# Performance work log

Measured on AMD Instinct MI355X. Metric: run time of the kernel, lower is better.

## Reference

```python
import math
import jax
import jax.numpy as jnp
import numpy as np

LMAX = 6                 # lmax
F8, F2 = 16, 64          # f_out//8, f_out//2 for f_out=128
DIM6 = sum((2 * l + 1) ** 2 for l in range(LMAX + 1))  # 455 = dim of so3_irreps(6)
NA = NB = NG = 16        # SO(3) activation grid (alpha, beta, gamma)
B, T, H, C = 32, 16, 4, 128


def _real_sh(lmax, xyz):
    # real spherical harmonics: (N,3) unit vectors -> (N,(lmax+1)^2), m=-l..l per l
    x, y, z = xyz[:, 0], xyz[:, 1], xyz[:, 2]
    st = np.sqrt(np.clip(1.0 - z * z, 0.0, None))
    phi = np.arctan2(y, x)
    n = xyz.shape[0]
    P = np.zeros((lmax + 1, lmax + 1, n))
    P[0, 0] = 1.0
    for m in range(1, lmax + 1):
        P[m, m] = -(2 * m - 1) * st * P[m - 1, m - 1]
    for m in range(lmax):
        P[m + 1, m] = (2 * m + 1) * z * P[m, m]
    for m in range(lmax + 1):
        for l in range(m + 2, lmax + 1):
            P[l, m] = ((2 * l - 1) * z * P[l - 1, m] - (l + m - 1) * P[l - 2, m]) / (l - m)
    cols = []
    for l in range(lmax + 1):
        for m in range(-l, l + 1):
            am = abs(m)
            K = math.sqrt((2 * l + 1) / (4 * math.pi) * math.factorial(l - am) / math.factorial(l + am))
            if m > 0:
                cols.append(math.sqrt(2.0) * K * np.cos(m * phi) * P[l, m])
            elif m < 0:
                cols.append(math.sqrt(2.0) * K * np.sin(am * phi) * P[l, am])
            else:
                cols.append(K * P[l, 0])
    return np.stack(cols, axis=-1)


def _flat_wigner(lmax, Rs):
    # component-normalized flat real Wigner-D basis: (G,3,3) -> (G, sum_l (2l+1)^2)
    # D_l(R) solved from Y_l(R x) = D_l(R) Y_l(x) by least squares in float64
    rng = np.random.default_rng(0)
    pts = rng.normal(size=(32, 3))
    pts /= np.linalg.norm(pts, axis=1, keepdims=True)
    Y = _real_sh(lmax, pts)                                     # (32,(lmax+1)^2)
    rp = np.einsum('gij,nj->gni', Rs, pts).reshape(-1, 3)
    Yr = _real_sh(lmax, rp).reshape(len(Rs), 32, -1)            # (G,32,(lmax+1)^2)
    blocks = []
    for l in range(lmax + 1):
        d = 2 * l + 1
        o = l * l
        Apinv = np.linalg.pinv(Y[:, o:o + d])                   # (d,32)
        D = np.einsum('kn,gnm->gmk', Apinv, Yr[:, :, o:o + d])  # (G,d,d)
        blocks.append(math.sqrt(d) * D.reshape(len(Rs), d * d))
    return np.concatenate(blocks, axis=-1)


def _rz(a):
    c, s = np.cos(a), np.sin(a)
    z, o = np.zeros_like(a), np.ones_like(a)
    return np.stack([np.stack([c, -s, z], -1), np.stack([s, c, z], -1), np.stack([z, z, o], -1)], -2)


def _ry(a):
    c, s = np.cos(a), np.sin(a)
    z, o = np.zeros_like(a), np.ones_like(a)
    return np.stack([np.stack([c, z, s], -1), np.stack([z, o, z], -1), np.stack([-s, z, c], -1)], -2)


def _so3_grid():
    # ZYZ Euler grid, Gauss-Legendre in beta; rotations (G,3,3) + Haar weights (G,) summing to 1
    nodes, wts = np.polynomial.legendre.leggauss(NB)
    betas = np.arccos(nodes)
    alphas = np.arange(NA) * 2 * np.pi / NA
    gammas = np.arange(NG) * 2 * np.pi / NG
    Aa, Bb, Cg = np.meshgrid(alphas, betas, gammas, indexing='ij')
    Rs = _rz(Aa.ravel()) @ _ry(Bb.ravel()) @ _rz(Cg.ravel())
    w = np.broadcast_to(wts[None, :, None], (NA, NB, NG)).ravel().copy()
    w *= (2 * np.pi / NA) * (2 * np.pi / NG) / (8 * np.pi ** 2)
    return Rs, w


def _ico_rotations():
    # the 60 rotations of the icosahedral group, generated by closure
    phi = (1.0 + 5.0 ** 0.5) / 2.0
    def rot(axis, ang):
        a = np.asarray(axis, dtype=np.float64)
        a = a / np.linalg.norm(a)
        K = np.array([[0.0, -a[2], a[1]], [a[2], 0.0, -a[0]], [-a[1], a[0], 0.0]])
        return np.eye(3) + math.sin(ang) * K + (1.0 - math.cos(ang)) * (K @ K)
    gens = [rot([0.0, 1.0, phi], 2.0 * np.pi / 5.0), rot([0.0, 0.0, 1.0], np.pi)]
    elems = [np.eye(3)]
    seen = {tuple(np.round(np.eye(3), 5).ravel())}
    frontier = list(elems)
    while frontier:
        nxt = []
        for R in frontier:
            for g in gens:
                Q = g @ R
                k = tuple(np.round(Q, 5).ravel())
                if k not in seen:
                    seen.add(k)
                    elems.append(Q)
                    nxt.append(Q)
        frontier = nxt
    return np.stack(elems)


def _equi_linear(xl, wl):
    # e3nn-style per-irrep linear: xl (...,f_in,u,m), wl (f_in,f_out,u,v); fan_in = f_in*u
    fan_in = wl.shape[0] * wl.shape[2]
    return jnp.einsum('...fum,fguv->...gvm', xl, wl) / np.sqrt(fan_in)


def _forward(x, trajectory, w1s, w1v, w2, D_in, D_outw, ico_wigners):
    b, t, _ = trajectory.shape
    # pack '1x0e+3x1e': scalar = traj[...,9], vectors = traj[...,:9]
    s = trajectory[..., 9][..., None, None, None]       # (b,t,f=1,u=1,m=1)
    v = trajectory[..., :9].reshape(b, t, 1, 3, 3)      # (b,t,f=1,u=3,m=3)
    h = jnp.concatenate([_equi_linear(s, w1s).reshape(b, t, F8, 1),
                         _equi_linear(v, w1v).reshape(b, t, F8, 9)], axis=-1)  # (b,t,16,10)
    # SO(3) activation: coeffs -> grid signal -> relu -> coeffs (lmax 1 -> 6)
    sig = jax.nn.relu(jnp.einsum('btci,gi->btcg', h, D_in))
    h = jnp.einsum('btcg,gi->btci', sig, D_outw)        # (b,t,16,455)
    # per-l equivariant linear, f 16 -> 64
    outs = []
    o = 0
    for l in range(LMAX + 1):
        d = 2 * l + 1
        xl = h[..., o:o + d * d].reshape(b, t, F8, d, d)
        outs.append(_equi_linear(xl, w2[l]).reshape(b, t, F2, d * d))
        o += d * d
    traj = jnp.concatenate(outs, axis=-1)               # (b,t,64,455)
    traj = jnp.einsum('bhcj,ij->bhci', traj, ico_wigners)  # sample on ico rotations
    xg = jnp.einsum('bhcj,ij->bhci', x, ico_wigners)
    return xg, traj


def setup_inputs():
    key = jax.random.key(0)
    ks = jax.random.split(key, 11)
    Rs, w = _so3_grid()
    D_in = _flat_wigner(1, Rs).astype(np.float32)                      # (G,10)
    D_outw = (_flat_wigner(LMAX, Rs) * w[:, None]).astype(np.float32)  # (G,455)
    ico = _flat_wigner(LMAX, _ico_rotations()).astype(np.float32)      # (60,455)
    inp = dict(
        x=jax.random.normal(ks[0], (B, H, C, DIM6), jnp.float32),
        trajectory=jax.random.normal(ks[1], (B, T, 10), jnp.float32),
        w1s=jax.random.normal(ks[2], (1, F8, 1, 1), jnp.float32),
        w1v=jax.random.normal(ks[3], (1, F8, 3, 3), jnp.float32),
        D_in=jnp.asarray(D_in),
        D_outw=jnp.asarray(D_outw),
        ico_wigners=jnp.asarray(ico),
    )
    for l in range(LMAX + 1):
        inp['w2_%d' % l] = jax.random.normal(ks[4 + l], (F8, F2, 2 * l + 1, 2 * l + 1), jnp.float32)
    return inp


def reference(x, trajectory, w1s, w1v, w2_0, w2_1, w2_2, w2_3, w2_4, w2_5, w2_6, D_in, D_outw, ico_wigners):
    w2 = [w2_0, w2_1, w2_2, w2_3, w2_4, w2_5, w2_6]
    return _forward(x, trajectory, w1s, w1v, w2, D_in, D_outw, ico_wigners)
```

## Files before the change

### kernel.cpp

```cpp
#include <hip/hip_runtime.h>
#include <math.h>


#define NBT  512
#define F8c  16
#define F2c  64
#define GJ   455
#define GG   4096
#define NICO 60
#define JP   512

typedef short bf16x8 __attribute__((ext_vector_type(8)));
typedef float f32x4  __attribute__((ext_vector_type(4)));
typedef unsigned int u32;
typedef unsigned short ushort;

struct W7 { const float* p[7]; };

__device__ __forceinline__ ushort f2bf(float f) {
  u32 u = __float_as_uint(f);
  return (ushort)((u + 0x7fffu + ((u >> 16) & 1u)) >> 16);
}

__device__ __forceinline__ int sel7(int l, int a0, int a1, int a2, int a3,
                                    int a4, int a5, int a6) {
  int r = a6;
  r = (l == 5) ? a5 : r; r = (l == 4) ? a4 : r; r = (l == 3) ? a3 : r;
  r = (l == 2) ? a2 : r; r = (l == 1) ? a1 : r; r = (l == 0) ? a0 : r;
  return r;
}
__device__ __forceinline__ float sel7f(int l, float a0, float a1, float a2,
                                       float a3, float a4, float a5, float a6) {
  float r = a6;
  r = (l == 5) ? a5 : r; r = (l == 4) ? a4 : r; r = (l == 3) ? a3 : r;
  r = (l == 2) ? a2 : r; r = (l == 1) ? a1 : r; r = (l == 0) ? a0 : r;
  return r;
}

__global__ __launch_bounds__(256) void k_pre(const float* __restrict__ traj,
                                             const float* __restrict__ w1s,
                                             const float* __restrict__ w1v,
                                             const float* __restrict__ ico,
                                             const float* __restrict__ Dout,
                                             W7 w2,
                                             float* __restrict__ h,
                                             ushort* __restrict__ icoB,
                                             ushort* __restrict__ icoBx,
                                             ushort* __restrict__ DoutBT,
                                             ushort* __restrict__ Abuf,
                                             ushort* __restrict__ Bbuf) {
  __shared__ float t[64][65];
  int b = blockIdx.x, tid = threadIdx.x;
  if (b < 2240) {
    ((uint4*)Abuf)[b * 256 + tid] = (uint4){0, 0, 0, 0};
  } else if (b < 2752) {
    int b2 = b - 2240;
    int jt = b2 & 7, kt = b2 >> 3;
    int tx = tid & 63, ty = tid >> 6;
    #pragma unroll
    for (int i = 0; i < 16; ++i) {
      int r = i * 4 + ty, j = jt * 64 + tx;
      t[r][tx] = (j < GJ) ? Dout[(size_t)(kt * 64 + r) * GJ + j] : 0.f;
    }
    __syncthreads();
    #pragma unroll
    for (int i = 0; i < 16; ++i) {
      int jl = i * 4 + ty;
      DoutBT[(size_t)(jt * 64 + jl) * GG + kt * 64 + tx] = f2bf(t[tx][jl]);
    }
  } else if (b < 4992) {
    int ee = (b - 2752) * 256 + tid;
    if (ee < 573440) {
      int l = (ee >= 4096) + (ee >= 16384) + (ee >= 57344) + (ee >= 114688) +
              (ee >= 225280) + (ee >= 360448);
      int base = sel7(l, 0, 4096, 16384, 57344, 114688, 225280, 360448);
      int d    = sel7(l, 1, 3, 5, 7, 9, 11, 13);
      int Kp   = sel7(l, 64, 64, 128, 128, 192, 192, 256);
      int local = ee - base;
      int row = local / Kp, kcol = local - row * Kp;
      int g2 = row / d, v = row - g2 * d;
      ushort val = 0;
      if (kcol < 16 * d) {
        int f = kcol / d, u = kcol - f * d;
        const float* wl = w2.p[l];
        float scl = rsqrtf(16.f * (float)d);
        val = f2bf(wl[(((size_t)f * 64 + g2) * d + u) * d + v] * scl);
      }
      Bbuf[ee] = val;
    }
  } else if (b < 5312) {
    int idx = (b - 4992) * 256 + tid;
    if (idx < NBT * 160) {
      int bt = idx / 160, r = idx % 160, c = r / 10, i = r % 10;
      const float* tr = traj + bt * 10;
      float val;
      if (i == 0) {
        val = tr[9] * w1s[c];
      } else {
        int k = i - 1, v = k / 3, m = k % 3;
        float s = 0.f;
        #pragma unroll
        for (int u = 0; u < 3; ++u) s = fmaf(tr[u * 3 + m], w1v[c * 9 + u * 3 + v], s);
        val = s * 0.57735026918962576f;
      }
      h[idx] = val;
    }
  } else if (b < 5440) {
    int e = (b - 5312) * 256 + tid;
    int i = e >> 9, k = e & 511;
    ushort val = 0;
    if (i < NICO && k < GJ) {
      int l = (k >= 1) + (k >= 10) + (k >= 35) + (k >= 84) + (k >= 165) + (k >= 286);
      int o = sel7(l, 0, 1, 10, 35, 84, 165, 286);
      int d = sel7(l, 1, 3, 5, 7, 9, 11, 13);
      float rcpd = sel7f(l, 1.f, 1.f / 3.f, 0.2f, 1.f / 7.f, 1.f / 9.f,
                         1.f / 11.f, 1.f / 13.f);
      int local = k - o;
      int m = (int)(((float)local + 0.5f) * rcpd);
      int v = local - m * d;
      val = f2bf(ico[i * GJ + o + v * d + m]);
    }
    icoB[e] = val;
  } else {
    int e = (b - 5440) * 256 + tid;
    int i = e >> 9, j = e & 511;
    icoBx[e] = (i < NICO && j < GJ) ? f2bf(ico[i * GJ + j]) : (ushort)0;
  }
}

__global__ __launch_bounds__(256) void k_sig(const float* __restrict__ h,
                                             const float* __restrict__ Din,
                                             ushort* __restrict__ sigb) {
  __shared__ float hs[160];
  int tid = threadIdx.x;
  int mb = blockIdx.y;
  int kt = blockIdx.x;
  if (tid < 160) hs[tid] = h[mb * 160 + tid];
  float dr[80];
  const float4* dp = (const float4*)(Din + (size_t)(kt * 2048 + tid * 8) * 10);
  #pragma unroll
  for (int q = 0; q < 20; ++q) {
    float4 v = dp[q];
    dr[q * 4 + 0] = v.x; dr[q * 4 + 1] = v.y; dr[q * 4 + 2] = v.z; dr[q * 4 + 3] = v.w;
  }
  __syncthreads();
  #pragma unroll
  for (int r = 0; r < 16; ++r) {
    float hv[10];
    #pragma unroll
    for (int i = 0; i < 10; ++i) hv[i] = hs[r * 10 + i];
    bf16x8 o;
    #pragma unroll
    for (int j = 0; j < 8; ++j) {
      float s = 0.f;
      #pragma unroll
      for (int i = 0; i < 10; ++i) s = fmaf(hv[i], dr[j * 10 + i], s);
      o[j] = (short)f2bf(fmaxf(s, 0.f));
    }
    *(bf16x8*)&sigb[((size_t)(mb * 16 + r)) * GG + kt * 2048 + tid * 8] = o;
  }
}

__global__ __launch_bounds__(256) void k_mm2s(const ushort* __restrict__ A,
                                              const ushort* __restrict__ Bm,
                                              float* __restrict__ part) {
  __shared__ __align__(16) short Asb[2][128 * 64];
  __shared__ __align__(16) short Bsb[2][128 * 64];
  int tid = threadIdx.x;
  int lane = tid & 63, wid = tid >> 6;
  int quad = lane >> 4, lr = lane & 15;
  int wm = wid >> 1, wn = wid & 1;
  int bid = blockIdx.x;
  int mb = bid & 63;
  int split = (bid >> 6) & 1;
  int nb = bid >> 7;
  int k0 = split * 2048;

  const ushort* Ab = A + (size_t)mb * 128 * GG + k0;
  const ushort* Bb = Bm + (size_t)nb * 128 * GG + k0;

  f32x4 acc[4][4];
  #pragma unroll
  for (int a = 0; a < 4; ++a)
    #pragma unroll
    for (int b = 0; b < 4; ++b) acc[a][b] = (f32x4){0.f, 0.f, 0.f, 0.f};

  auto stage = [&](int buf, int kc) {
    #pragma unroll
    for (int it = 0; it < 4; ++it) {
      int s0 = (wid * 4 + it) * 64;
      int s = s0 + lane;
      int r = s >> 3, pp = s & 7, p = pp ^ (r & 7);
      __builtin_amdgcn_global_load_lds(
          (const __attribute__((address_space(1))) u32*)(Ab + (size_t)r * GG + kc + p * 8),
          (__attribute__((address_space(3))) u32*)(&Asb[buf][s0 * 8]), 16, 0, 0);
    }
    #pragma unroll
    for (int it = 0; it < 4; ++it) {
      int s0 = (wid * 4 + it) * 64;
      int s = s0 + lane;
      int r = s >> 3, pp = s & 7, p = pp ^ (r & 7);
      __builtin_amdgcn_global_load_lds(
          (const __attribute__((address_space(1))) u32*)(Bb + (size_t)r * GG + kc + p * 8),
          (__attribute__((address_space(3))) u32*)(&Bsb[buf][s0 * 8]), 16, 0, 0);
    }
  };

  stage(0, 0);
  __syncthreads();
  for (int it = 0; it < 32; ++it) {
    int cur = it & 1;
    if (it < 31) stage(cur ^ 1, (it + 1) * 64);
    #pragma unroll
    for (int ks = 0; ks < 2; ++ks) {
      bf16x8 af[4], bv[4];
      #pragma unroll
      for (int mt = 0; mt < 4; ++mt) {
        int ra = wm * 64 + mt * 16 + lr;
        int v = (ks * 4 + quad) ^ (ra & 7);
        af[mt] = *(const bf16x8*)&Asb[cur][(ra * 8 + v) * 8];
      }
      #pragma unroll
      for (int nt = 0; nt < 4; ++nt) {
        int rb = wn * 64 + nt * 16 + lr;
        int v = (ks * 4 + quad) ^ (rb & 7);
        bv[nt] = *(const bf16x8*)&Bsb[cur][(rb * 8 + v) * 8];
      }
      #pragma unroll
      for (int mt = 0; mt < 4; ++mt)
        #pragma unroll
        for (int nt = 0; nt < 4; ++nt)
          acc[mt][nt] = __builtin_amdgcn_mfma_f32_16x16x32_bf16(af[mt], bv[nt], acc[mt][nt], 0, 0, 0);
    }
    __syncthreads();
  }
  #pragma unroll
  for (int mt = 0; mt < 4; ++mt)
    #pragma unroll
    for (int nt = 0; nt < 4; ++nt) {
      int j = nb * 128 + wn * 64 + nt * 16 + lr;
      #pragma unroll
      for (int r = 0; r < 4; ++r) {
        int m = mb * 128 + wm * 64 + mt * 16 + quad * 4 + r;
        part[((size_t)split * 8192 + m) * 512 + j] = acc[mt][nt][r];
      }
    }
}

__global__ __launch_bounds__(256) void k_red(const float* __restrict__ part,
                                             ushort* __restrict__ Abuf) {
  int t = blockIdx.x * 256 + threadIdx.x;
  int e0 = t * 8;
  int m = e0 >> 9, j0 = e0 & 511;
  const float4* p0 = (const float4*)(part + (size_t)m * 512 + j0);
  const float4* p1 = (const float4*)(part + (size_t)(8192 + m) * 512 + j0);
  float4 a0 = p0[0], a1 = p0[1], b0 = p1[0], b1 = p1[1];
  float s[8] = {a0.x + b0.x, a0.y + b0.y, a0.z + b0.z, a0.w + b0.w,
                a1.x + b1.x, a1.y + b1.y, a1.z + b1.z, a1.w + b1.w};
  int btg = m >> 4, f = m & 15;
  #pragma unroll
  for (int jj = 0; jj < 8; ++jj) {
    int j = j0 + jj;
    if (j < GJ) {
      int l = (j >= 1) + (j >= 10) + (j >= 35) + (j >= 84) + (j >= 165) + (j >= 286);
      int o    = sel7(l, 0, 1, 10, 35, 84, 165, 286);
      int d    = sel7(l, 1, 3, 5, 7, 9, 11, 13);
      int Kp   = sel7(l, 64, 64, 128, 128, 192, 192, 256);
      int Aoff = sel7(l, 0, 32768, 131072, 458752, 917504, 1802240, 2883584);
      float rcpd = sel7f(l, 1.f, 1.f / 3.f, 0.2f, 1.f / 7.f, 1.f / 9.f,
                         1.f / 11.f, 1.f / 13.f);
      int jl = j - o;
      int u = (int)(((float)jl + 0.5f) * rcpd);
      int mB = jl - u * d;
      Abuf[(size_t)Aoff + ((size_t)btg * d + mB) * Kp + f * d + u] = f2bf(s[jj]);
    }
  }
}

__global__ __launch_bounds__(256) void k_mm2f(const ushort* __restrict__ A,
                                              const ushort* __restrict__ Bm,
                                              ushort* __restrict__ Abuf) {
  __shared__ __align__(16) short Asb[2][128 * 64];
  __shared__ __align__(16) short Bsb[2][128 * 64];
  int tid = threadIdx.x;
  int lane = tid & 63, wid = tid >> 6;
  int quad = lane >> 4, lr = lane & 15;
  int wm = wid >> 1, wn = wid & 1;
  int bid = blockIdx.x;
  int mb = bid & 63, nb = bid >> 6;
  f32x4 acc[4][4];
  #pragma unroll
  for (int a = 0; a < 4; ++a)
    #pragma unroll
    for (int b = 0; b < 4; ++b) acc[a][b] = (f32x4){0.f, 0.f, 0.f, 0.f};
  const ushort* Ab = A + (size_t)mb * 128 * GG;
  const ushort* Bb = Bm + (size_t)nb * 128 * GG;
  auto stage = [&](int buf, int kc) {
    #pragma unroll
    for (int it = 0; it < 4; ++it) {
      int s0 = (wid * 4 + it) * 64;
      int s = s0 + lane;
      int r = s >> 3, pp = s & 7, p = pp ^ (r & 7);
      __builtin_amdgcn_global_load_lds(
          (const __attribute__((address_space(1))) u32*)(Ab + (size_t)r * GG + kc + p * 8),
          (__attribute__((address_space(3))) u32*)(&Asb[buf][s0 * 8]), 16, 0, 0);
    }
    #pragma unroll
    for (int it = 0; it < 4; ++it) {
      int s0 = (wid * 4 + it) * 64;
      int s = s0 + lane;
      int r = s >> 3, pp = s & 7, p = pp ^ (r & 7);
      __builtin_amdgcn_global_load_lds(
          (const __attribute__((address_space(1))) u32*)(Bb + (size_t)r * GG + kc + p * 8),
          (__attribute__((address_space(3))) u32*)(&Bsb[buf][s0 * 8]), 16, 0, 0);
    }
  };
  stage(0, 0);
  __syncthreads();
  for (int it = 0; it < 64; ++it) {
    int cur = it & 1;
    if (it < 63) stage(cur ^ 1, (it + 1) * 64);
    #pragma unroll
    for (int ks = 0; ks < 2; ++ks) {
      bf16x8 af[4], bvv[4];
      #pragma unroll
      for (int mt = 0; mt < 4; ++mt) {
        int ra = wm * 64 + mt * 16 + lr;
        int v = (ks * 4 + quad) ^ (ra & 7);
        af[mt] = *(const bf16x8*)&Asb[cur][(ra * 8 + v) * 8];
      }
      #pragma unroll
      for (int nt = 0; nt < 4; ++nt) {
        int rb = wn * 64 + nt * 16 + lr;
        int v = (ks * 4 + quad) ^ (rb & 7);
        bvv[nt] = *(const bf16x8*)&Bsb[cur][(rb * 8 + v) * 8];
      }
      #pragma unroll
      for (int mt = 0; mt < 4; ++mt)
        #pragma unroll
        for (int nt = 0; nt < 4; ++nt)
          acc[mt][nt] = __builtin_amdgcn_mfma_f32_16x16x32_bf16(af[mt], bvv[nt], acc[mt][nt], 0, 0, 0);
    }
    __syncthreads();
  }
  #pragma unroll
  for (int nt = 0; nt < 4; ++nt) {
    int j = nb * 128 + wn * 64 + nt * 16 + lr;
    if (j < GJ) {
      int l = (j >= 1) + (j >= 10) + (j >= 35) + (j >= 84) + (j >= 165) + (j >= 286);
      int o    = sel7(l, 0, 1, 10, 35, 84, 165, 286);
      int d    = sel7(l, 1, 3, 5, 7, 9, 11, 13);
      int Kp   = sel7(l, 64, 64, 128, 128, 192, 192, 256);
      int Aoff = sel7(l, 0, 32768, 131072, 458752, 917504, 1802240, 2883584);
      int jl = j - o;
      float rcpd = 1.0f / (float)d;
      int u = (int)(((float)jl + 0.5f) * rcpd);
      int mB = jl - u * d;
      #pragma unroll
      for (int mt = 0; mt < 4; ++mt)
        #pragma unroll
        for (int r = 0; r < 4; ++r) {
          int m = mb * 128 + wm * 64 + mt * 16 + quad * 4 + r;
          int btg = m >> 4, f = m & 15;
          Abuf[(size_t)Aoff + ((size_t)btg * d + mB) * Kp + f * d + u] =
              f2bf(acc[mt][nt][r]);
        }
    }
  }
}

__global__ __launch_bounds__(256) void k_batchX(const ushort* __restrict__ Abuf,
                                                const ushort* __restrict__ Bbuf,
                                                const float* __restrict__ x,
                                                const ushort* __restrict__ icoBx,
                                                ushort* __restrict__ trajbf,
                                                float* __restrict__ xg) {
  __shared__ __align__(16) short As[2][64 * 64];
  __shared__ __align__(16) short Bs[2][64 * 64];
  int bid = blockIdx.x;
  int tid = threadIdx.x;
  int lane = tid & 63, wid = tid >> 6;
  int quad = lane >> 4, lr = lane & 15;
  int wm = wid >> 1, wn = wid & 1;
  f32x4 acc[2][2];
  #pragma unroll
  for (int a = 0; a < 2; ++a)
    #pragma unroll
    for (int b = 0; b < 2; ++b) acc[a][b] = (f32x4){0.f, 0.f, 0.f, 0.f};

  auto compute = [&](int cur) {
    #pragma unroll
    for (int ks = 0; ks < 2; ++ks) {
      int v = (ks * 4 + quad) ^ (lr & 7);
      bf16x8 af[2], bfv[2];
      #pragma unroll
      for (int mt = 0; mt < 2; ++mt)
        af[mt] = *(const bf16x8*)&As[cur][(wm * 32 + mt * 16 + lr) * 64 + v * 8];
      #pragma unroll
      for (int nt = 0; nt < 2; ++nt)
        bfv[nt] = *(const bf16x8*)&Bs[cur][(wn * 32 + nt * 16 + lr) * 64 + v * 8];
      #pragma unroll
      for (int mt = 0; mt < 2; ++mt)
        #pragma unroll
        for (int nt = 0; nt < 2; ++nt)
          acc[mt][nt] = __builtin_amdgcn_mfma_f32_16x16x32_bf16(af[mt], bfv[nt], acc[mt][nt], 0, 0, 0);
    }
  };

  if (bid >= 3640) {
    int mtile = bid - 3640;
    auto loadx = [&](int itk, float* xv) {
      #pragma unroll
      for (int half = 0; half < 2; ++half) {
        int s = half * 256 + tid;
        int r = s >> 3, p8 = s & 7, p = p8 ^ (r & 7);
        const float* xr = x + (size_t)(mtile * 64 + r) * GJ;
        int j0 = itk * 64 + p * 8;
        #pragma unroll
        for (int jj = 0; jj < 8; ++jj) {
          int j = j0 + jj;
          xv[half * 8 + jj] = (j < GJ) ? xr[j] : 0.f;
        }
      }
    };
    auto writex = [&](int buf, const float* xv) {
      #pragma unroll
      for (int half = 0; half < 2; ++half) {
        int s = half * 256 + tid;
        bf16x8 v8;
        #pragma unroll
        for (int jj = 0; jj < 8; ++jj) v8[jj] = (short)f2bf(xv[half * 8 + jj]);
        *(bf16x8*)&As[buf][s * 8] = v8;
      }
    };
    auto stageB = [&](int buf, int kc) {
      #pragma unroll
      for (int it = 0; it < 2; ++it) {
        int s0 = (wid * 2 + it) * 64;
        int s = s0 + lane;
        int r = s >> 3, p8 = s & 7, p = p8 ^ (r & 7);
        const ushort* gb = icoBx + (size_t)r * JP + kc + p * 8;
        __builtin_amdgcn_global_load_lds(
            (const __attribute__((address_space(1))) u32*)gb,
            (__attribute__((address_space(3))) u32*)(&Bs[buf][s0 * 8]), 16, 0, 0);
      }
    };
    float xv[16];
    loadx(0, xv);
    writex(0, xv);
    stageB(0, 0);
    __syncthreads();
    for (int it = 0; it < 8; ++it) {
      int cur = it & 1;
      float xn[16];
      if (it < 7) {
        loadx(it + 1, xn);
        stageB(cur ^ 1, (it + 1) * 64);
      }
      compute(cur);
      if (it < 7) writex(cur ^ 1, xn);
      __syncthreads();
    }
    #pragma unroll
    for (int mt = 0; mt < 2; ++mt)
      #pragma unroll
      for (int nt = 0; nt < 2; ++nt) {
        int i = wn * 32 + nt * 16 + lr;
        if (i < NICO) {
          #pragma unroll
          for (int r = 0; r < 4; ++r) {
            int row = mtile * 64 + wm * 32 + mt * 16 + quad * 4 + r;
            xg[(size_t)row * NICO + i] = acc[mt][nt][r];
          }
        }
      }
    return;
  }

  int l = (bid >= 8) + (bid >= 80) + (bid >= 280) + (bid >= 672) +
          (bid >= 1320) + (bid >= 2288);
  int bbase = sel7(l, 0, 8, 80, 280, 672, 1320, 2288);
  int d     = sel7(l, 1, 3, 5, 7, 9, 11, 13);
  int Kp    = sel7(l, 64, 64, 128, 128, 192, 192, 256);
  int o     = sel7(l, 0, 1, 10, 35, 84, 165, 286);
  int Aoff  = sel7(l, 0, 32768, 131072, 458752, 917504, 1802240, 2883584);
  int Boff  = sel7(l, 0, 4096, 16384, 57344, 114688, 225280, 360448);
  int t = bid - bbase;
  float rcp8d = sel7f(l, 1.f / 8.f, 1.f / 24.f, 1.f / 40.f, 1.f / 56.f,
                      1.f / 72.f, 1.f / 88.f, 1.f / 104.f);
  int ntile = (int)(((float)t + 0.5f) * rcp8d);
  int mtile = t - ntile * 8 * d;

  const ushort* Ab = Abuf + Aoff;
  const ushort* Bb = Bbuf + Boff;

  auto stage = [&](int buf, int kc) {
    #pragma unroll
    for (int it = 0; it < 2; ++it) {
      int s0 = (wid * 2 + it) * 64;
      int s = s0 + lane;
      int r = s >> 3, p8 = s & 7, p = p8 ^ (r & 7);
      const ushort* ga = Ab + (size_t)(mtile * 64 + r) * Kp + kc + p * 8;
      __builtin_amdgcn_global_load_lds(
          (const __attribute__((address_space(1))) u32*)ga,
          (__attribute__((address_space(3))) u32*)(&As[buf][s0 * 8]), 16, 0, 0);
      const ushort* gb = Bb + (size_t)(ntile * 64 + r) * Kp + kc + p * 8;
      __builtin_amdgcn_global_load_lds(
          (const __attribute__((address_space(1))) u32*)gb,
          (__attribute__((address_space(3))) u32*)(&Bs[buf][s0 * 8]), 16, 0, 0);
    }
  };

  int nIter = Kp >> 6;
  stage(0, 0);
  __syncthreads();
  for (int it = 0; it < nIter; ++it) {
    int cur = it & 1;
    if (it + 1 < nIter) stage(cur ^ 1, (it + 1) * 64);
    compute(cur);
    __syncthreads();
  }
  #pragma unroll
  for (int mt = 0; mt < 2; ++mt)
    #pragma unroll
    for (int nt = 0; nt < 2; ++nt)
      #pragma unroll
      for (int r = 0; r < 4; ++r) {
        int Mrow = mtile * 64 + wm * 32 + mt * 16 + quad * 4 + r;
        int Ncol = ntile * 64 + wn * 32 + nt * 16 + lr;
        int bt = Mrow / d, m = Mrow - bt * d;
        int g2 = Ncol / d, v = Ncol - g2 * d;
        trajbf[(size_t)(bt * 64 + g2) * JP + o + m * d + v] = f2bf(acc[mt][nt][r]);
      }
}

__global__ __launch_bounds__(256) void k_icoT(const ushort* __restrict__ trajbf,
                                              const ushort* __restrict__ icoB,
                                              float* __restrict__ trajo) {
  __shared__ __align__(16) short As[2][64 * 64];
  __shared__ __align__(16) short Bs[2][64 * 64];
  int mtile = blockIdx.x;
  int tid = threadIdx.x;
  int lane = tid & 63, wid = tid >> 6;
  int quad = lane >> 4, lr = lane & 15;
  int wm = wid >> 1, wn = wid & 1;
  f32x4 acc[2][2];
  #pragma unroll
  for (int a = 0; a < 2; ++a)
    #pragma unroll
    for (int b = 0; b < 2; ++b) acc[a][b] = (f32x4){0.f, 0.f, 0.f, 0.f};

  auto stage = [&](int buf, int kc) {
    #pragma unroll
    for (int it = 0; it < 2; ++it) {
      int s0 = (wid * 2 + it) * 64;
      int s = s0 + lane;
      int r = s >> 3, p8 = s & 7, p = p8 ^ (r & 7);
      const ushort* ga = trajbf + (size_t)(mtile * 64 + r) * JP + kc + p * 8;
      __builtin_amdgcn_global_load_lds(
          (const __attribute__((address_space(1))) u32*)ga,
          (__attribute__((address_space(3))) u32*)(&As[buf][s0 * 8]), 16, 0, 0);
      const ushort* gb = icoB + (size_t)r * JP + kc + p * 8;
      __builtin_amdgcn_global_load_lds(
          (const __attribute__((address_space(1))) u32*)gb,
          (__attribute__((address_space(3))) u32*)(&Bs[buf][s0 * 8]), 16, 0, 0);
    }
  };

  stage(0, 0);
  __syncthreads();
  for (int it = 0; it < 8; ++it) {
    int cur = it & 1;
    if (it < 7) stage(cur ^ 1, (it + 1) * 64);
    #pragma unroll
    for (int ks = 0; ks < 2; ++ks) {
      int v = (ks * 4 + quad) ^ (lr & 7);
      bf16x8 af[2], bfv[2];
      #pragma unroll
      for (int mt = 0; mt < 2; ++mt)
        af[mt] = *(const bf16x8*)&As[cur][(wm * 32 + mt * 16 + lr) * 64 + v * 8];
      #pragma unroll
      for (int nt = 0; nt < 2; ++nt)
        bfv[nt] = *(const bf16x8*)&Bs[cur][(wn * 32 + nt * 16 + lr) * 64 + v * 8];
      #pragma unroll
      for (int mt = 0; mt < 2; ++mt)
        #pragma unroll
        for (int nt = 0; nt < 2; ++nt)
          acc[mt][nt] = __builtin_amdgcn_mfma_f32_16x16x32_bf16(af[mt], bfv[nt], acc[mt][nt], 0, 0, 0);
    }
    __syncthreads();
  }
  #pragma unroll
  for (int mt = 0; mt < 2; ++mt)
    #pragma unroll
    for (int nt = 0; nt < 2; ++nt) {
      int i = wn * 32 + nt * 16 + lr;
      if (i < NICO) {
        #pragma unroll
        for (int r = 0; r < 4; ++r) {
          int row = mtile * 64 + wm * 32 + mt * 16 + quad * 4 + r;
          trajo[(size_t)row * NICO + i] = acc[mt][nt][r];
        }
      }
    }
}

extern "C" void kernel_launch(void* const* d_in, const int* in_sizes, int n_in,
                              void* d_out, int out_size, void* d_ws, size_t ws_size,
                              hipStream_t stream) {
  const float *x = nullptr, *traj = nullptr, *w1s = nullptr, *w1v = nullptr;
  const float *Din = nullptr, *Dout = nullptr, *ico = nullptr;
  W7 w2{};
  for (int i = 0; i < n_in; ++i) {
    const float* p = (const float*)d_in[i];
    switch (in_sizes[i]) {
      case 7454720: x = p; break;
      case 5120:    traj = p; break;
      case 16:      w1s = p; break;
      case 144:     w1v = p; break;
      case 40960:   Din = p; break;
      case 1863680: Dout = p; break;
      case 27300:   ico = p; break;
      case 1024:    w2.p[0] = p; break;
      case 9216:    w2.p[1] = p; break;
      case 25600:   w2.p[2] = p; break;
      case 50176:   w2.p[3] = p; break;
      case 82944:   w2.p[4] = p; break;
      case 123904:  w2.p[5] = p; break;
      case 173056:  w2.p[6] = p; break;
      default: break;
    }
  }
  char* wsb = (char*)d_ws;
  float*  h       = (float*)wsb;
  ushort* DoutBT  = (ushort*)(wsb + 327680);
  ushort* icoB    = (ushort*)(wsb + 4521984);
  ushort* icoBx   = (ushort*)(wsb + 4587520);
  ushort* Abuf    = (ushort*)(wsb + 4653056);
  ushort* Bbuf    = (ushort*)(wsb + 13828096);
  ushort* sigb    = (ushort*)(wsb + 14974976);
  ushort* trajbf  = sigb;
  float*  part    = (float*)(wsb + 82083840);
  float* xg    = (float*)d_out;
  float* trajo = (float*)d_out + 983040;

  k_pre<<<dim3(5568), dim3(256), 0, stream>>>(traj, w1s, w1v, ico, Dout, w2,
                                              h, icoB, icoBx, DoutBT, Abuf, Bbuf);
  k_sig<<<dim3(2, 512), dim3(256), 0, stream>>>(h, Din, sigb);
  if (ws_size >= 115638272ULL) {
    k_mm2s<<<dim3(512),  dim3(256), 0, stream>>>(sigb, DoutBT, part);
    k_red <<<dim3(2048), dim3(256), 0, stream>>>(part, Abuf);
  } else {
    k_mm2f<<<dim3(256),  dim3(256), 0, stream>>>(sigb, DoutBT, Abuf);
  }
  k_batchX<<<dim3(3896), dim3(256), 0, stream>>>(Abuf, Bbuf, x, icoBx, trajbf, xg);
  k_icoT  <<<dim3(512),  dim3(256), 0, stream>>>(trajbf, icoB, trajo);
}
```

Measured before the change: 232.7 us.

## Enlarge GEMM tiles to 128-wide in batchX and icoT kernels

Grows the per-block GEMM tiles from 64x64 to 128x128 in the per-l batched matmuls, and to 128x64 in the x-projection and ico GEMMs, so each wave holds a 4x4 or 4x2 MFMA accumulator array. Block counts and the per-l tile index maps change to match, and the output remap now uses float reciprocal division with an N-boundary guard. The aim is more operand reuse per LDS load and fewer blocks and redundant global reads. The cost is more registers and LDS per block, lower occupancy, and fewer blocks to fill the GPU, especially in icoT with 256 blocks.

```diff
diff --git a/kernel.cpp b/kernel.cpp
--- a/kernel.cpp
+++ b/kernel.cpp
@@ -375,65 +375,46 @@
                                                 const ushort* __restrict__ icoBx,
                                                 ushort* __restrict__ trajbf,
                                                 float* __restrict__ xg) {
-  __shared__ __align__(16) short As[2][64 * 64];
-  __shared__ __align__(16) short Bs[2][64 * 64];
+  __shared__ __align__(16) short As[2][128 * 64];
+  __shared__ __align__(16) short Bs[2][128 * 64];
   int bid = blockIdx.x;
   int tid = threadIdx.x;
   int lane = tid & 63, wid = tid >> 6;
   int quad = lane >> 4, lr = lane & 15;
   int wm = wid >> 1, wn = wid & 1;
-  f32x4 acc[2][2];
-  #pragma unroll
-  for (int a = 0; a < 2; ++a)
-    #pragma unroll
-    for (int b = 0; b < 2; ++b) acc[a][b] = (f32x4){0.f, 0.f, 0.f, 0.f};
-
-  auto compute = [&](int cur) {
-    #pragma unroll
-    for (int ks = 0; ks < 2; ++ks) {
-      int v = (ks * 4 + quad) ^ (lr & 7);
-      bf16x8 af[2], bfv[2];
-      #pragma unroll
-      for (int mt = 0; mt < 2; ++mt)
-        af[mt] = *(const bf16x8*)&As[cur][(wm * 32 + mt * 16 + lr) * 64 + v * 8];
-      #pragma unroll
-      for (int nt = 0; nt < 2; ++nt)
-        bfv[nt] = *(const bf16x8*)&Bs[cur][(wn * 32 + nt * 16 + lr) * 64 + v * 8];
-      #pragma unroll
-      for (int mt = 0; mt < 2; ++mt)
-        #pragma unroll
-        for (int nt = 0; nt < 2; ++nt)
-          acc[mt][nt] = __builtin_amdgcn_mfma_f32_16x16x32_bf16(af[mt], bfv[nt], acc[mt][nt], 0, 0, 0);
-    }
-  };
-
-  if (bid >= 3640) {
-    int mtile = bid - 3640;
+  f32x4 acc[4][4];
+  #pragma unroll
+  for (int a = 0; a < 4; ++a)
+    #pragma unroll
+    for (int b = 0; b < 4; ++b) acc[a][b] = (f32x4){0.f, 0.f, 0.f, 0.f};
+
+  if (bid >= 1008) {
+    int mtile = bid - 1008;
     auto loadx = [&](int itk, float* xv) {
       #pragma unroll
-      for (int half = 0; half < 2; ++half) {
-        int s = half * 256 + tid;
+      for (int g = 0; g < 4; ++g) {
+        int s = g * 256 + tid;
         int r = s >> 3, p8 = s & 7, p = p8 ^ (r & 7);
-        const float* xr = x + (size_t)(mtile * 64 + r) * GJ;
+        const float* xr = x + (size_t)(mtile * 128 + r) * GJ;
         int j0 = itk * 64 + p * 8;
         #pragma unroll
         for (int jj = 0; jj < 8; ++jj) {
           int j = j0 + jj;
-          xv[half * 8 + jj] = (j < GJ) ? xr[j] : 0.f;
+          xv[g * 8 + jj] = (j < GJ) ? xr[j] : 0.f;
         }
       }
     };
     auto writex = [&](int buf, const float* xv) {
       #pragma unroll
-      for (int half = 0; half < 2; ++half) {
-        int s = half * 256 + tid;
+      for (int g = 0; g < 4; ++g) {
+        int s = g * 256 + tid;
         bf16x8 v8;
         #pragma unroll
-        for (int jj = 0; jj < 8; ++jj) v8[jj] = (short)f2bf(xv[half * 8 + jj]);
+        for (int jj = 0; jj < 8; ++jj) v8[jj] = (short)f2bf(xv[g * 8 + jj]);
         *(bf16x8*)&As[buf][s * 8] = v8;
       }
     };
-    auto stageB = [&](int buf, int kc) {
+    auto stageBx = [&](int buf, int kc) {
       #pragma unroll
       for (int it = 0; it < 2; ++it) {
         int s0 = (wid * 2 + it) * 64;
@@ -445,31 +426,51 @@
             (__attribute__((address_space(3))) u32*)(&Bs[buf][s0 * 8]), 16, 0, 0);
       }
     };
-    float xv[16];
+    float xv[32];
     loadx(0, xv);
     writex(0, xv);
-    stageB(0, 0);
+    stageBx(0, 0);
     __syncthreads();
     for (int it = 0; it < 8; ++it) {
       int cur = it & 1;
-      float xn[16];
+      float xn[32];
       if (it < 7) {
         loadx(it + 1, xn);
-        stageB(cur ^ 1, (it + 1) * 64);
-      }
-      compute(cur);
+        stageBx(cur ^ 1, (it + 1) * 64);
+      }
+      #pragma unroll
+      for (int ks = 0; ks < 2; ++ks) {
+        bf16x8 af[4], bv[2];
+        #pragma unroll
+        for (int mt = 0; mt < 4; ++mt) {
+          int ra = wm * 64 + mt * 16 + lr;
+          int v = (ks * 4 + quad) ^ (ra & 7);
+          af[mt] = *(const bf16x8*)&As[cur][(ra * 8 + v) * 8];
+        }
+        #pragma unroll
+        for (int nt = 0; nt < 2; ++nt) {
+          int rb = wn * 32 + nt * 16 + lr;
+          int v = (ks * 4 + quad) ^ (rb & 7);
+          bv[nt] = *(const bf16x8*)&Bs[cur][(rb * 8 + v) * 8];
+        }
+        #pragma unroll
+        for (int mt = 0; mt < 4; ++mt)
+          #pragma unroll
+          for (int nt = 0; nt < 2; ++nt)
+            acc[mt][nt] = __builtin_amdgcn_mfma_f32_16x16x32_bf16(af[mt], bv[nt], acc[mt][nt], 0, 0, 0);
+      }
       if (it < 7) writex(cur ^ 1, xn);
       __syncthreads();
     }
     #pragma unroll
-    for (int mt = 0; mt < 2; ++mt)
+    for (int mt = 0; mt < 4; ++mt)
       #pragma unroll
       for (int nt = 0; nt < 2; ++nt) {
         int i = wn * 32 + nt * 16 + lr;
         if (i < NICO) {
           #pragma unroll
           for (int r = 0; r < 4; ++r) {
-            int row = mtile * 64 + wm * 32 + mt * 16 + quad * 4 + r;
+            int row = mtile * 128 + wm * 64 + mt * 16 + quad * 4 + r;
             xg[(size_t)row * NICO + i] = acc[mt][nt][r];
           }
         }
@@ -477,36 +478,43 @@
     return;
   }
 
-  int l = (bid >= 8) + (bid >= 80) + (bid >= 280) + (bid >= 672) +
-          (bid >= 1320) + (bid >= 2288);
-  int bbase = sel7(l, 0, 8, 80, 280, 672, 1320, 2288);
+  int l = (bid >= 4) + (bid >= 28) + (bid >= 88) + (bid >= 200) +
+          (bid >= 380) + (bid >= 644);
+  int bbase = sel7(l, 0, 4, 28, 88, 200, 380, 644);
   int d     = sel7(l, 1, 3, 5, 7, 9, 11, 13);
   int Kp    = sel7(l, 64, 64, 128, 128, 192, 192, 256);
   int o     = sel7(l, 0, 1, 10, 35, 84, 165, 286);
   int Aoff  = sel7(l, 0, 32768, 131072, 458752, 917504, 1802240, 2883584);
   int Boff  = sel7(l, 0, 4096, 16384, 57344, 114688, 225280, 360448);
+  int ntc   = sel7(l, 1, 2, 3, 4, 5, 6, 7);
+  float rcpntc = sel7f(l, 1.f, 0.5f, 1.f / 3.f, 0.25f, 0.2f, 1.f / 6.f, 1.f / 7.f);
+  float rcpd   = sel7f(l, 1.f, 1.f / 3.f, 0.2f, 1.f / 7.f, 1.f / 9.f,
+                       1.f / 11.f, 1.f / 13.f);
   int t = bid - bbase;
-  float rcp8d = sel7f(l, 1.f / 8.f, 1.f / 24.f, 1.f / 40.f, 1.f / 56.f,
-                      1.f / 72.f, 1.f / 88.f, 1.f / 104.f);
-  int ntile = (int)(((float)t + 0.5f) * rcp8d);
-  int mtile = t - ntile * 8 * d;
-
-  const ushort* Ab = Abuf + Aoff;
-  const ushort* Bb = Bbuf + Boff;
+  int mtile = (int)(((float)t + 0.5f) * rcpntc);
+  int ntile = t - mtile * ntc;
+  int Nl = 64 * d;
+
+  const ushort* Ab = Abuf + Aoff + (size_t)mtile * 128 * Kp;
+  const ushort* Bb = Bbuf + Boff + (size_t)ntile * 128 * Kp;
 
   auto stage = [&](int buf, int kc) {
     #pragma unroll
-    for (int it = 0; it < 2; ++it) {
-      int s0 = (wid * 2 + it) * 64;
+    for (int it = 0; it < 4; ++it) {
+      int s0 = (wid * 4 + it) * 64;
       int s = s0 + lane;
-      int r = s >> 3, p8 = s & 7, p = p8 ^ (r & 7);
-      const ushort* ga = Ab + (size_t)(mtile * 64 + r) * Kp + kc + p * 8;
+      int r = s >> 3, pp = s & 7, p = pp ^ (r & 7);
       __builtin_amdgcn_global_load_lds(
-          (const __attribute__((address_space(1))) u32*)ga,
+          (const __attribute__((address_space(1))) u32*)(Ab + (size_t)r * Kp + kc + p * 8),
           (__attribute__((address_space(3))) u32*)(&As[buf][s0 * 8]), 16, 0, 0);
-      const ushort* gb = Bb + (size_t)(ntile * 64 + r) * Kp + kc + p * 8;
+    }
+    #pragma unroll
+    for (int it = 0; it < 4; ++it) {
+      int s0 = (wid * 4 + it) * 64;
+      int s = s0 + lane;
+      int r = s >> 3, pp = s & 7, p = pp ^ (r & 7);
       __builtin_amdgcn_global_load_lds(
-          (const __attribute__((address_space(1))) u32*)gb,
+          (const __attribute__((address_space(1))) u32*)(Bb + (size_t)r * Kp + kc + p * 8),
           (__attribute__((address_space(3))) u32*)(&Bs[buf][s0 * 8]), 16, 0, 0);
     }
   };
@@ -517,49 +525,80 @@
   for (int it = 0; it < nIter; ++it) {
     int cur = it & 1;
     if (it + 1 < nIter) stage(cur ^ 1, (it + 1) * 64);
-    compute(cur);
+    #pragma unroll
+    for (int ks = 0; ks < 2; ++ks) {
+      bf16x8 af[4], bv[4];
+      #pragma unroll
+      for (int mt = 0; mt < 4; ++mt) {
+        int ra = wm * 64 + mt * 16 + lr;
+        int v = (ks * 4 + quad) ^ (ra & 7);
+        af[mt] = *(const bf16x8*)&As[cur][(ra * 8 + v) * 8];
+      }
+      #pragma unroll
+      for (int nt = 0; nt < 4; ++nt) {
+        int rb = wn * 64 + nt * 16 + lr;
+        int v = (ks * 4 + quad) ^ (rb & 7);
+        bv[nt] = *(const bf16x8*)&Bs[cur][(rb * 8 + v) * 8];
+      }
+      #pragma unroll
+      for (int mt = 0; mt < 4; ++mt)
+        #pragma unroll
+        for (int nt = 0; nt < 4; ++nt)
+          acc[mt][nt] = __builtin_amdgcn_mfma_f32_16x16x32_bf16(af[mt], bv[nt], acc[mt][nt], 0, 0, 0);
+    }
     __syncthreads();
   }
   #pragma unroll
-  for (int mt = 0; mt < 2; ++mt)
-    #pragma unroll
-    for (int nt = 0; nt < 2; ++nt)
-      #pragma unroll
-      for (int r = 0; r < 4; ++r) {
-        int Mrow = mtile * 64 + wm * 32 + mt * 16 + quad * 4 + r;
-        int Ncol = ntile * 64 + wn * 32 + nt * 16 + lr;
-        int bt = Mrow / d, m = Mrow - bt * d;
-        int g2 = Ncol / d, v = Ncol - g2 * d;
-        trajbf[(size_t)(bt * 64 + g2) * JP + o + m * d + v] = f2bf(acc[mt][nt][r]);
-      }
+  for (int nt = 0; nt < 4; ++nt) {
+    int Ncol = ntile * 128 + wn * 64 + nt * 16 + lr;
+    if (Ncol < Nl) {
+      int g2 = (int)(((float)Ncol + 0.5f) * rcpd);
+      int v = Ncol - g2 * d;
+      #pragma unroll
+      for (int mt = 0; mt < 4; ++mt)
+        #pragma unroll
+        for (int r = 0; r < 4; ++r) {
+          int Mrow = mtile * 128 + wm * 64 + mt * 16 + quad * 4 + r;
+          int bt = (int)(((float)Mrow + 0.5f) * rcpd);
+          int m = Mrow - bt * d;
+          trajbf[(size_t)(bt * 64 + g2) * JP + o + m * d + v] = f2bf(acc[mt][nt][r]);
+        }
+    }
+  }
 }
 
 __global__ __launch_bounds__(256) void k_icoT(const ushort* __restrict__ trajbf,
                                               const ushort* __restrict__ icoB,
                                               float* __restrict__ trajo) {
-  __shared__ __align__(16) short As[2][64 * 64];
+  __shared__ __align__(16) short As[2][128 * 64];
   __shared__ __align__(16) short Bs[2][64 * 64];
   int mtile = blockIdx.x;
   int tid = threadIdx.x;
   int lane = tid & 63, wid = tid >> 6;
   int quad = lane >> 4, lr = lane & 15;
   int wm = wid >> 1, wn = wid & 1;
-  f32x4 acc[2][2];
-  #pragma unroll
-  for (int a = 0; a < 2; ++a)
+  f32x4 acc[4][2];
+  #pragma unroll
+  for (int a = 0; a < 4; ++a)
     #pragma unroll
     for (int b = 0; b < 2; ++b) acc[a][b] = (f32x4){0.f, 0.f, 0.f, 0.f};
 
   auto stage = [&](int buf, int kc) {
+    #pragma unroll
+    for (int it = 0; it < 4; ++it) {
+      int s0 = (wid * 4 + it) * 64;
+      int s = s0 + lane;
+      int r = s >> 3, p8 = s & 7, p = p8 ^ (r & 7);
+      const ushort* ga = trajbf + (size_t)(mtile * 128 + r) * JP + kc + p * 8;
+      __builtin_amdgcn_global_load_lds(
+          (const __attribute__((address_space(1))) u32*)ga,
+          (__attribute__((address_space(3))) u32*)(&As[buf][s0 * 8]), 16, 0, 0);
+    }
     #pragma unroll
     for (int it = 0; it < 2; ++it) {
       int s0 = (wid * 2 + it) * 64;
       int s = s0 + lane;
       int r = s >> 3, p8 = s & 7, p = p8 ^ (r & 7);
-      const ushort* ga = trajbf + (size_t)(mtile * 64 + r) * JP + kc + p * 8;
-      __builtin_amdgcn_global_load_lds(
-          (const __attribute__((address_space(1))) u32*)ga,
-          (__attribute__((address_space(3))) u32*)(&As[buf][s0 * 8]), 16, 0, 0);
       const ushort* gb = icoB + (size_t)r * JP + kc + p * 8;
       __builtin_amdgcn_global_load_lds(
           (const __attribute__((address_space(1))) u32*)gb,
@@ -574,31 +613,36 @@
     if (it < 7) stage(cur ^ 1, (it + 1) * 64);
     #pragma unroll
     for (int ks = 0; ks < 2; ++ks) {
-      int v = (ks * 4 + quad) ^ (lr & 7);
-      bf16x8 af[2], bfv[2];
-      #pragma unroll
-      for (int mt = 0; mt < 2; ++mt)
-        af[mt] = *(const bf16x8*)&As[cur][(wm * 32 + mt * 16 + lr) * 64 + v * 8];
-      #pragma unroll
-      for (int nt = 0; nt < 2; ++nt)
-        bfv[nt] = *(const bf16x8*)&Bs[cur][(wn * 32 + nt * 16 + lr) * 64 + v * 8];
-      #pragma unroll
-      for (int mt = 0; mt < 2; ++mt)
+      bf16x8 af[4], bv[2];
+      #pragma unroll
+      for (int mt = 0; mt < 4; ++mt) {
+        int ra = wm * 64 + mt * 16 + lr;
+        int v = (ks * 4 + quad) ^ (ra & 7);
+        af[mt] = *(const bf16x8*)&As[cur][(ra * 8 + v) * 8];
+      }
+      #pragma unroll
+      for (int nt = 0; nt < 2; ++nt) {
+        int rb = wn * 32 + nt * 16 + lr;
+        int v = (ks * 4 + quad) ^ (rb & 7);
+        bv[nt] = *(const bf16x8*)&Bs[cur][(rb * 8 + v) * 8];
+      }
+      #pragma unroll
+      for (int mt = 0; mt < 4; ++mt)
         #pragma unroll
         for (int nt = 0; nt < 2; ++nt)
-          acc[mt][nt] = __builtin_amdgcn_mfma_f32_16x16x32_bf16(af[mt], bfv[nt], acc[mt][nt], 0, 0, 0);
+          acc[mt][nt] = __builtin_amdgcn_mfma_f32_16x16x32_bf16(af[mt], bv[nt], acc[mt][nt], 0, 0, 0);
     }
     __syncthreads();
   }
   #pragma unroll
-  for (int mt = 0; mt < 2; ++mt)
+  for (int mt = 0; mt < 4; ++mt)
     #pragma unroll
     for (int nt = 0; nt < 2; ++nt) {
       int i = wn * 32 + nt * 16 + lr;
       if (i < NICO) {
         #pragma unroll
         for (int r = 0; r < 4; ++r) {
-          int row = mtile * 64 + wm * 32 + mt * 16 + quad * 4 + r;
+          int row = mtile * 128 + wm * 64 + mt * 16 + quad * 4 + r;
           trajo[(size_t)row * NICO + i] = acc[mt][nt][r];
         }
       }
@@ -653,6 +697,6 @@
   } else {
     k_mm2f<<<dim3(256),  dim3(256), 0, stream>>>(sigb, DoutBT, Abuf);
   }
-  k_batchX<<<dim3(3896), dim3(256), 0, stream>>>(Abuf, Bbuf, x, icoBx, trajbf, xg);
-  k_icoT  <<<dim3(512),  dim3(256), 0, stream>>>(trajbf, icoB, trajo);
-}
+  k_batchX<<<dim3(1136), dim3(256), 0, stream>>>(Abuf, Bbuf, x, icoBx, trajbf, xg);
+  k_icoT  <<<dim3(256),  dim3(256), 0, stream>>>(trajbf, icoB, trajo);
+}
```

After: 236.0 us. About the same (+1.4%).
